# Performance work log

Hardware: AMD Instinct MI355X
Metric: run time of the kernel (lower is better)

## Reference

```python
import jax, jax.numpy as jnp
import numpy as np

N_HEAD, D_MODEL, D_HEAD = 16, 1024, 64
QLEN, BSZ = 1024, 8
LN_EPS = 1e-5


def _rel_shift(x):
    # x: [b, n, i, j]; Transformer-XL relative shift via pad/reshape/slice
    b, n, i, j = x.shape
    x = jnp.pad(x, ((0, 0), (0, 0), (0, 0), (1, 0)))  # [b,n,i,j+1]
    x = x.reshape(b, n, j + 1, i)[:, :, 1:, :].reshape(b, n, i, j)
    return x


def setup_inputs() -> dict:
    key = jax.random.key(0)
    k = jax.random.split(key, 8)
    w = jax.random.normal(k[0], (QLEN, BSZ, D_MODEL), dtype=jnp.float32)
    r_emb = jax.random.normal(k[1], (QLEN, N_HEAD, D_HEAD), dtype=jnp.float32) * 0.02
    r_w_bias = jax.random.normal(k[2], (N_HEAD, D_HEAD), dtype=jnp.float32) * 0.02
    r_bias = jax.random.normal(k[3], (QLEN, N_HEAD), dtype=jnp.float32) * 0.02
    # causal mask: True means masked (j > i)
    attn_mask = jnp.triu(jnp.ones((QLEN, QLEN), dtype=bool), k=1)
    qkv_w = jax.random.normal(k[4], (D_MODEL, 3 * N_HEAD * D_HEAD), dtype=jnp.float32) * (D_MODEL ** -0.5)
    o_w = jax.random.normal(k[5], (N_HEAD * D_HEAD, D_MODEL), dtype=jnp.float32) * ((N_HEAD * D_HEAD) ** -0.5)
    ln_g = jnp.ones((D_MODEL,), dtype=jnp.float32)
    ln_b = jnp.zeros((D_MODEL,), dtype=jnp.float32)
    return {"w": w, "r_emb": r_emb, "r_w_bias": r_w_bias, "r_bias": r_bias,
            "qkv_w": qkv_w, "o_w": o_w, "ln_g": ln_g, "ln_b": ln_b,
            "attn_mask": attn_mask}


def reference(w, r_emb, r_w_bias, r_bias, qkv_w, o_w, ln_g, ln_b, attn_mask):
    qlen, bsz, d_model = w.shape
    n_head, d_head = r_w_bias.shape
    scale = 1.0 / (d_head ** 0.5)

    heads = w @ qkv_w  # [q, b, 3*H*D]
    q_h, k_h, v_h = jnp.split(heads, 3, axis=-1)
    q_h = q_h.reshape(qlen, bsz, n_head, d_head)
    k_h = k_h.reshape(qlen, bsz, n_head, d_head)
    v_h = v_h.reshape(qlen, bsz, n_head, d_head)

    # klen == qlen (no mems), r_emb/r_bias already length klen
    rw_q = q_h + r_w_bias[None, None]                      # [i,b,n,d]
    AC = jnp.einsum('ibnd,jbnd->bnij', rw_q, k_h)          # content score
    B_ = jnp.einsum('ibnd,jnd->bnij', q_h, r_emb)          # position score
    D_ = r_bias.T[None, :, None, :]                        # [1,n,1,j]
    BD = _rel_shift(B_ + D_)
    attn_score = scale * (AC + BD)                         # [b,n,i,j]

    attn_score = jnp.where(attn_mask[None, None], -jnp.inf, attn_score)
    attn_prob = jax.nn.softmax(attn_score, axis=3)

    attn_vec = jnp.einsum('bnij,jbnd->ibnd', attn_prob, v_h)
    attn_vec = attn_vec.reshape(qlen, bsz, n_head * d_head)
    attn_out = attn_vec @ o_w

    # post-LN residual
    y = w + attn_out
    mu = jnp.mean(y, axis=-1, keepdims=True)
    var = jnp.mean((y - mu) ** 2, axis=-1, keepdims=True)
    out = (y - mu) * jax.lax.rsqrt(var + LN_EPS) * ln_g + ln_b
    return out
```

## Files before the change

kernel.cpp:

```cpp
#include <hip/hip_runtime.h>

typedef unsigned short u16;
typedef __attribute__((ext_vector_type(8))) short bf16x8;
typedef __attribute__((ext_vector_type(4))) short bf16x4;
typedef __attribute__((ext_vector_type(4))) float f32x4;
typedef __attribute__((ext_vector_type(4))) unsigned short u16x4;
typedef __attribute__((ext_vector_type(2))) unsigned int u32x2;

#define SEQ 1024
#define BSZ 8
#define NHD 16
#define DHD 64
#define DMODEL 1024

__device__ __forceinline__ u16 f2bf(float x) {
  unsigned u = __float_as_uint(x);
  return (u16)((u + 0x7fffu + ((u >> 16) & 1u)) >> 16);
}
__device__ __forceinline__ float bf2f(u16 h) {
  return __uint_as_float(((unsigned)h) << 16);
}

typedef const __attribute__((address_space(1))) unsigned int gu32_t;
typedef __attribute__((address_space(3))) unsigned int lu32_t;
__device__ __forceinline__ void gload16(const void* g, void* l) {
  __builtin_amdgcn_global_load_lds((gu32_t*)g, (lu32_t*)l, 16, 0, 0);
}

__global__ void cast_w_k(const float* __restrict__ in, u16* __restrict__ out) {
  size_t i = ((size_t)blockIdx.x * 256 + threadIdx.x) * 4;
  float4 v = *(const float4*)(in + i);
  u16x4 o;
  o[0] = f2bf(v.x); o[1] = f2bf(v.y); o[2] = f2bf(v.z); o[3] = f2bf(v.w);
  *(u16x4*)(out + i) = o;
}

__global__ void transpose_cast_k(const float* __restrict__ in, u16* __restrict__ out,
                                 int R, int C) {
  __shared__ float tile[32][33];
  int tx = threadIdx.x & 31, ty = threadIdx.x >> 5;
  int bx = blockIdx.x * 32, by = blockIdx.y * 32;
#pragma unroll
  for (int rr = ty; rr < 32; rr += 8)
    tile[rr][tx] = in[(size_t)(by + rr) * C + bx + tx];
  __syncthreads();
#pragma unroll
  for (int rr = ty; rr < 32; rr += 8)
    out[(size_t)(bx + rr) * R + by + tx] = f2bf(tile[tx][rr]);
}

__global__ void cast_remb_k(const float* __restrict__ in, u16* __restrict__ out) {
  int t0 = blockIdx.x * 256 + threadIdx.x;
  int jn = t0 >> 3, db = t0 & 7;
  int j = jn >> 4, n = jn & 15;
  const float* src = in + (size_t)jn * 64 + db * 8;
  u16* dst = out + (size_t)n * 65536 + (size_t)(j >> 4) * 1024 + (db >> 2) * 512 +
             (((j & 15) | ((db & 3) << 4)) << 3);
#pragma unroll
  for (int e = 0; e < 8; ++e) dst[e] = f2bf(src[e]);
}

__global__ void cvec_k(const float* __restrict__ remb, const float* __restrict__ rwb,
                       float* __restrict__ cv) {
  int idx = blockIdx.x * 256 + threadIdx.x;
  int n = idx >> 10, t = idx & 1023;
  const float* src = remb + (size_t)(t * 16 + n) * 64;
  const float* wb = rwb + n * 64;
  float s = 0.f;
#pragma unroll
  for (int d = 0; d < 64; ++d) s += src[d] * wb[d];
  cv[idx] = s;
}

template <int EPI>
__global__ __launch_bounds__(256) void gemm_bt(
    const u16* __restrict__ A, const u16* __restrict__ Bt, int K, int nbn,
    u16* __restrict__ q_o, u16* __restrict__ k_o, u16* __restrict__ v_o,
    const float* __restrict__ resid, float* __restrict__ yout) {
  __shared__ __attribute__((aligned(16))) u16 ldsA[2][4096];
  __shared__ __attribute__((aligned(16))) u16 ldsB[2][4096];
  const int tid = threadIdx.x;
  const int wid = tid >> 6, l = tid & 63;
  const int l15 = l & 15, lg = l >> 4;
  const int cpx = gridDim.x >> 3;
  const int id0 = blockIdx.x;
  const int lid = (id0 & 7) * cpx + (id0 >> 3);
  const int bm = lid / nbn, bn = lid % nbn;
  const int wm = wid & 1, wn = wid >> 1;
  const size_t ldb = (size_t)K * 2;

  const char* aA = (const char*)A + (size_t)(bm * 128 + wid * 32 + (l >> 2)) * ldb + (l & 3) * 16;
  const char* aB = (const char*)Bt + (size_t)(bn * 128 + wid * 32 + (l >> 2)) * ldb + (l & 3) * 16;

  auto stage = [&](int buf, int kt) {
    const char* sa = aA + (size_t)kt * 64;
    const char* sb = aB + (size_t)kt * 64;
    char* la = (char*)&ldsA[buf][wid * 1024];
    char* lb = (char*)&ldsB[buf][wid * 1024];
    gload16(sa, la);
    gload16(sa + 16 * ldb, la + 1024);
    gload16(sb, lb);
    gload16(sb + 16 * ldb, lb + 1024);
  };

  f32x4 acc[4][4] = {};
  stage(0, 0);
  __syncthreads();
  const int NT = K >> 5;
  for (int t = 0; t < NT; ++t) {
    int cur = t & 1;
    if (t + 1 < NT) stage(cur ^ 1, t + 1);
    bf16x8 af[4], bfr[4];
#pragma unroll
    for (int mi = 0; mi < 4; ++mi)
      af[mi] = *(const bf16x8*)&ldsA[cur][(wm * 64 + mi * 16 + l15) * 32 + lg * 8];
#pragma unroll
    for (int ni = 0; ni < 4; ++ni)
      bfr[ni] = *(const bf16x8*)&ldsB[cur][(wn * 64 + ni * 16 + l15) * 32 + lg * 8];
#pragma unroll
    for (int mi = 0; mi < 4; ++mi)
#pragma unroll
      for (int ni = 0; ni < 4; ++ni)
        acc[mi][ni] = __builtin_amdgcn_mfma_f32_16x16x32_bf16(af[mi], bfr[ni], acc[mi][ni], 0, 0, 0);
    __syncthreads();
  }

  if (EPI == 0) {
#pragma unroll
    for (int mi = 0; mi < 4; ++mi)
#pragma unroll
      for (int ni = 0; ni < 4; ++ni) {
        int c = bn * 128 + wn * 64 + ni * 16 + l15;
        int which = c >> 10, rem = c & 1023, h = rem >> 6, d = rem & 63;
        u16* dst = which == 0 ? q_o : (which == 1 ? k_o : v_o);
#pragma unroll
        for (int r = 0; r < 4; ++r) {
          int rg = bm * 128 + wm * 64 + mi * 16 + lg * 4 + r;
          int i = rg >> 3, bb = rg & 7;
          int bn2 = bb * 16 + h;
          size_t idx;
          if (which == 0) {
            idx = ((size_t)bn2 * 1024 + i) * 64 + d;
          } else if (which == 1) {
            idx = (size_t)bn2 * 65536 + (size_t)(i >> 4) * 1024 + (d >> 5) * 512 +
                  (((i & 15) | (((d >> 3) & 3) << 4)) << 3) + (d & 7);
          } else {
            idx = (size_t)bn2 * 65536 + (size_t)(i >> 4) * 1024 + (d >> 4) * 256 +
                  (((d & 15) | (((i >> 2) & 3) << 4)) << 2) + (i & 3);
          }
          dst[idx] = f2bf(acc[mi][ni][r]);
        }
      }
  } else {
#pragma unroll
    for (int mi = 0; mi < 4; ++mi)
#pragma unroll
      for (int ni = 0; ni < 4; ++ni) {
        int c = bn * 128 + wn * 64 + ni * 16 + l15;
#pragma unroll
        for (int r = 0; r < 4; ++r) {
          int rg = bm * 128 + wm * 64 + mi * 16 + lg * 4 + r;
          size_t off = (size_t)rg * 1024 + c;
          yout[off] = resid[off] + acc[mi][ni][r];
        }
      }
  }
}

__global__ __launch_bounds__(256, 3) void attn_k(
    const u16* __restrict__ qg, const u16* __restrict__ kf, const u16* __restrict__ vf,
    const u16* __restrict__ rf, const float* __restrict__ rbias,
    const float* __restrict__ cvec, const float* __restrict__ rwb,
    u16* __restrict__ av) {
  __shared__ __attribute__((aligned(16))) u16 EldsA[4][16][84];
  __shared__ __attribute__((aligned(16))) u16 EldsB[4][16][84];
  __shared__ __attribute__((aligned(16))) float rb[1088];

  const int tid = threadIdx.x;
  const int wid = tid >> 6, l = tid & 63;
  const int l15 = l & 15, lg = l >> 4;
  const int id = blockIdx.x;
  const int qblk = 7 - (id >> 7);
  const int n = (id & 7) | (((id >> 3) & 1) << 3);
  const int b = (id >> 4) & 7;
  const int bn = b * 16 + n;
  const int ib = qblk * 128;
  const int iw = ib + wid * 32;

  const float SC = 0.18033688011f;

  for (int idx = tid; idx < 1088; idx += 256)
    rb[idx] = (idx < 1024) ? (SC * (rbias[idx * 16 + n] - cvec[n * 1024 + idx]) - 16.0f)
                           : -1e30f;

  const float* wbp = rwb + n * 64;
  const u16* qrowA = qg + ((size_t)bn * 1024 + iw + l15) * 64;
  const u16* qrowB = qrowA + 16 * 64;
  bf16x8 qa0 = *(const bf16x8*)(qrowA + lg * 8);
  bf16x8 qa1 = *(const bf16x8*)(qrowA + 32 + lg * 8);
  bf16x8 qb0 = *(const bf16x8*)(qrowB + lg * 8);
  bf16x8 qb1 = *(const bf16x8*)(qrowB + 32 + lg * 8);
  bf16x8 qwA0, qwA1, qwB0, qwB1;
#pragma unroll
  for (int e = 0; e < 8; ++e) {
    float w0 = wbp[lg * 8 + e], w1 = wbp[32 + lg * 8 + e];
    qwA0[e] = (short)f2bf(SC * (bf2f((u16)qa0[e]) + w0));
    qwA1[e] = (short)f2bf(SC * (bf2f((u16)qa1[e]) + w1));
    qwB0[e] = (short)f2bf(SC * (bf2f((u16)qb0[e]) + w0));
    qwB1[e] = (short)f2bf(SC * (bf2f((u16)qb1[e]) + w1));
  }

  f32x4 oaccA[4] = {}, oaccB[4] = {};
  float lpA = 0.f, lpB = 0.f;

  const u16* kfp = kf + (size_t)bn * 65536 + l * 8;
  const u16* vfp = vf + (size_t)bn * 65536 + l * 4;
  const u16* rfp = rf + (size_t)n * 65536 + l * 8;

  __syncthreads();

  const int njt = (iw >> 6) + 1;
  for (int jt = 0; jt < njt; ++jt) {
    const int jb = jt * 64;

    const u16* kt = kfp + jt * 4096;
    bf16x8 kk[8];
#pragma unroll
    for (int s = 0; s < 8; ++s) kk[s] = *(const bf16x8*)(kt + s * 512);

    const int tbB = jb - iw - 16 + 1008;
    const int t16b = tbB >> 4;
#pragma unroll
    for (int f = 0; f < 6; ++f) {
      int t16 = t16b + f;
      if (t16 > 63) t16 = 63;
      const u16* rr = rfp + t16 * 1024;
      bf16x8 ra0 = *(const bf16x8*)(rr);
      bf16x8 ra1 = *(const bf16x8*)(rr + 512);
      f32x4 rb4 = *(const f32x4*)&rb[tbB + f * 16 + lg * 4];
      if (f < 5) {
        f32x4 et = {};
        et = __builtin_amdgcn_mfma_f32_16x16x32_bf16(ra0, qwB0, et, 0, 0, 0);
        et = __builtin_amdgcn_mfma_f32_16x16x32_bf16(ra1, qwB1, et, 0, 0, 0);
        et = et + rb4;
        unsigned lo, hi;
        asm("v_cvt_pk_bf16_f32 %0, %1, %2" : "=v"(lo) : "v"(et[0]), "v"(et[1]));
        asm("v_cvt_pk_bf16_f32 %0, %1, %2" : "=v"(hi) : "v"(et[2]), "v"(et[3]));
        u32x2 t2; t2[0] = lo; t2[1] = hi;
        *(u32x2*)&EldsB[wid][l15][f * 16 + lg * 4] = t2;
      }
      if (f >= 1) {
        f32x4 et = {};
        et = __builtin_amdgcn_mfma_f32_16x16x32_bf16(ra0, qwA0, et, 0, 0, 0);
        et = __builtin_amdgcn_mfma_f32_16x16x32_bf16(ra1, qwA1, et, 0, 0, 0);
        et = et + rb4;
        unsigned lo, hi;
        asm("v_cvt_pk_bf16_f32 %0, %1, %2" : "=v"(lo) : "v"(et[0]), "v"(et[1]));
        asm("v_cvt_pk_bf16_f32 %0, %1, %2" : "=v"(hi) : "v"(et[2]), "v"(et[3]));
        u32x2 t2; t2[0] = lo; t2[1] = hi;
        *(u32x2*)&EldsA[wid][l15][(f - 1) * 16 + lg * 4] = t2;
      }
    }

    f32x4 stA[4], stB[4];
    __builtin_amdgcn_s_setprio(1);
#pragma unroll
    for (int jj = 0; jj < 4; ++jj) {
      f32x4 a = __builtin_amdgcn_mfma_f32_16x16x32_bf16(kk[jj * 2], qwA0, (f32x4){}, 0, 0, 0);
      stA[jj] = __builtin_amdgcn_mfma_f32_16x16x32_bf16(kk[jj * 2 + 1], qwA1, a, 0, 0, 0);
    }
#pragma unroll
    for (int jj = 0; jj < 4; ++jj) {
      f32x4 a = __builtin_amdgcn_mfma_f32_16x16x32_bf16(kk[jj * 2], qwB0, (f32x4){}, 0, 0, 0);
      stB[jj] = __builtin_amdgcn_mfma_f32_16x16x32_bf16(kk[jj * 2 + 1], qwB1, a, 0, 0, 0);
    }
    __builtin_amdgcn_s_setprio(0);

    const u16* vt0 = vfp + jt * 4096;
    bf16x4 vv[4][4];
#pragma unroll
    for (int jj = 0; jj < 4; ++jj)
#pragma unroll
      for (int dd = 0; dd < 4; ++dd)
        vv[jj][dd] = *(const bf16x4*)(vt0 + jj * 1024 + dd * 256);

    bf16x4 paA[4], paB[4];
#pragma unroll
    for (int jj = 0; jj < 4; ++jj) {
      const int ebase = jj * 16 + lg * 4 - l15 + 15;
      {
        float v0 = stA[jj][0] + bf2f(EldsA[wid][l15][ebase + 0]);
        float v1 = stA[jj][1] + bf2f(EldsA[wid][l15][ebase + 1]);
        float v2 = stA[jj][2] + bf2f(EldsA[wid][l15][ebase + 2]);
        float v3 = stA[jj][3] + bf2f(EldsA[wid][l15][ebase + 3]);
        float p0, p1, p2, p3;
        asm("v_exp_f32 %0, %1" : "=v"(p0) : "v"(v0));
        asm("v_exp_f32 %0, %1" : "=v"(p1) : "v"(v1));
        asm("v_exp_f32 %0, %1" : "=v"(p2) : "v"(v2));
        asm("v_exp_f32 %0, %1" : "=v"(p3) : "v"(v3));
        lpA += (p0 + p1) + (p2 + p3);
        unsigned lo, hi;
        asm("v_cvt_pk_bf16_f32 %0, %1, %2" : "=v"(lo) : "v"(p0), "v"(p1));
        asm("v_cvt_pk_bf16_f32 %0, %1, %2" : "=v"(hi) : "v"(p2), "v"(p3));
        u32x2 t2; t2[0] = lo; t2[1] = hi;
        paA[jj] = __builtin_bit_cast(bf16x4, t2);
      }
      {
        float v0 = stB[jj][0] + bf2f(EldsB[wid][l15][ebase + 0]);
        float v1 = stB[jj][1] + bf2f(EldsB[wid][l15][ebase + 1]);
        float v2 = stB[jj][2] + bf2f(EldsB[wid][l15][ebase + 2]);
        float v3 = stB[jj][3] + bf2f(EldsB[wid][l15][ebase + 3]);
        float p0, p1, p2, p3;
        asm("v_exp_f32 %0, %1" : "=v"(p0) : "v"(v0));
        asm("v_exp_f32 %0, %1" : "=v"(p1) : "v"(v1));
        asm("v_exp_f32 %0, %1" : "=v"(p2) : "v"(v2));
        asm("v_exp_f32 %0, %1" : "=v"(p3) : "v"(v3));
        lpB += (p0 + p1) + (p2 + p3);
        unsigned lo, hi;
        asm("v_cvt_pk_bf16_f32 %0, %1, %2" : "=v"(lo) : "v"(p0), "v"(p1));
        asm("v_cvt_pk_bf16_f32 %0, %1, %2" : "=v"(hi) : "v"(p2), "v"(p3));
        u32x2 t2; t2[0] = lo; t2[1] = hi;
        paB[jj] = __builtin_bit_cast(bf16x4, t2);
      }
    }

    __builtin_amdgcn_s_setprio(1);
#pragma unroll
    for (int dd = 0; dd < 4; ++dd)
#pragma unroll
      for (int jj = 0; jj < 4; ++jj)
        oaccA[dd] = __builtin_amdgcn_mfma_f32_16x16x16bf16_1k(paA[jj], vv[jj][dd], oaccA[dd], 0, 0, 0);
#pragma unroll
    for (int dd = 0; dd < 4; ++dd)
#pragma unroll
      for (int jj = 0; jj < 4; ++jj)
        oaccB[dd] = __builtin_amdgcn_mfma_f32_16x16x16bf16_1k(paB[jj], vv[jj][dd], oaccB[dd], 0, 0, 0);
    __builtin_amdgcn_s_setprio(0);
  }

  lpA += __shfl_xor(lpA, 16);
  lpA += __shfl_xor(lpA, 32);
  lpB += __shfl_xor(lpB, 16);
  lpB += __shfl_xor(lpB, 32);
  float liA = 1.f / lpA, liB = 1.f / lpB;
  float ioA[4], ioB[4];
#pragma unroll
  for (int r2 = 0; r2 < 4; ++r2) {
    ioA[r2] = __shfl(liA, (l & 48) | (lg * 4 + r2));
    ioB[r2] = __shfl(liB, (l & 48) | (lg * 4 + r2));
  }
#pragma unroll
  for (int dd = 0; dd < 4; ++dd)
#pragma unroll
    for (int r2 = 0; r2 < 4; ++r2) {
      int igA = iw + lg * 4 + r2;
      av[((size_t)igA * 8 + b) * 1024 + n * 64 + dd * 16 + l15] = f2bf(oaccA[dd][r2] * ioA[r2]);
      int igB = igA + 16;
      av[((size_t)igB * 8 + b) * 1024 + n * 64 + dd * 16 + l15] = f2bf(oaccB[dd][r2] * ioB[r2]);
    }
}

__global__ void ln_k(float* __restrict__ y, const float* __restrict__ g,
                     const float* __restrict__ be) {
  const int row = blockIdx.x, tid = threadIdx.x;
  float* p = y + (size_t)row * 1024;
  float4 v = ((const float4*)p)[tid];
  float s1 = v.x + v.y + v.z + v.w;
  float s2 = v.x * v.x + v.y * v.y + v.z * v.z + v.w * v.w;
#pragma unroll
  for (int mk = 1; mk < 64; mk <<= 1) {
    s1 += __shfl_xor(s1, mk);
    s2 += __shfl_xor(s2, mk);
  }
  __shared__ float as1[4], as2[4];
  if ((tid & 63) == 0) { as1[tid >> 6] = s1; as2[tid >> 6] = s2; }
  __syncthreads();
  s1 = as1[0] + as1[1] + as1[2] + as1[3];
  s2 = as2[0] + as2[1] + as2[2] + as2[3];
  float mu = s1 * (1.f / 1024.f);
  float var = s2 * (1.f / 1024.f) - mu * mu;
  float rs = rsqrtf(var + 1e-5f);
  float4 gg = ((const float4*)g)[tid];
  float4 bb = ((const float4*)be)[tid];
  float4 o;
  o.x = (v.x - mu) * rs * gg.x + bb.x;
  o.y = (v.y - mu) * rs * gg.y + bb.y;
  o.z = (v.z - mu) * rs * gg.z + bb.z;
  o.w = (v.w - mu) * rs * gg.w + bb.w;
  ((float4*)p)[tid] = o;
}

extern "C" void kernel_launch(void* const* d_in, const int* in_sizes, int n_in,
                              void* d_out, int out_size, void* d_ws, size_t ws_size,
                              hipStream_t stream) {
  (void)in_sizes; (void)n_in; (void)out_size; (void)ws_size;
  const float* w      = (const float*)d_in[0];
  const float* r_emb  = (const float*)d_in[1];
  const float* r_wb   = (const float*)d_in[2];
  const float* r_bias = (const float*)d_in[3];
  const float* qkv_w  = (const float*)d_in[4];
  const float* o_w    = (const float*)d_in[5];
  const float* ln_g   = (const float*)d_in[6];
  const float* ln_b   = (const float*)d_in[7];
  float* out = (float*)d_out;
  char* ws = (char*)d_ws;

  u16* w_b    = (u16*)(ws + 0);
  u16* qkvw_t = (u16*)(ws + 16777216);
  u16* ow_t   = (u16*)(ws + 23068672);
  u16* remb_f = (u16*)(ws + 25165824);
  u16* q_b    = (u16*)(ws + 27262976);
  u16* k_f    = (u16*)(ws + 44040192);
  u16* v_f    = (u16*)(ws + 60817408);
  float* cvb  = (float*)(ws + 77594624);
  u16* av_b   = w_b;

  cast_w_k<<<8192, 256, 0, stream>>>(w, w_b);
  transpose_cast_k<<<dim3(96, 32), 256, 0, stream>>>(qkv_w, qkvw_t, 1024, 3072);
  transpose_cast_k<<<dim3(32, 32), 256, 0, stream>>>(o_w, ow_t, 1024, 1024);
  cast_remb_k<<<512, 256, 0, stream>>>(r_emb, remb_f);
  cvec_k<<<64, 256, 0, stream>>>(r_emb, r_wb, cvb);
  gemm_bt<0><<<dim3(1536), 256, 0, stream>>>(w_b, qkvw_t, 1024, 24, q_b, k_f, v_f, nullptr, nullptr);
  attn_k<<<dim3(1024), 256, 0, stream>>>(q_b, k_f, v_f, remb_f, r_bias, cvb, r_wb, av_b);
  gemm_bt<1><<<dim3(512), 256, 0, stream>>>(av_b, ow_t, 1024, 8, nullptr, nullptr, nullptr, w, out);
  ln_k<<<8192, 256, 0, stream>>>(out, ln_g, ln_b);
}
```

Measured before the change: 199.4 us.

## Fuse preprocessing kernels into one launch and halve attention block size

Merges the five preprocessing kernels (w cast, two weight transpose-casts, r_emb relayout, cvec dot products) into a single launch that dispatches on block index, cutting launch overhead and inter-kernel gaps. The attention kernel now uses 128-thread blocks covering 64 query rows with 2048 blocks instead of 256 threads over 128 rows. The smaller blocks give finer load balance across the causal triangle and more resident blocks, but each block redoes the r_bias table setup, and the hidden body must handle two waves correctly.

```diff
diff --git a/kernel.cpp b/kernel.cpp
--- a/kernel.cpp
+++ b/kernel.cpp
@@ -27,49 +27,56 @@
   __builtin_amdgcn_global_load_lds((gu32_t*)g, (lu32_t*)l, 16, 0, 0);
 }
 
-__global__ void cast_w_k(const float* __restrict__ in, u16* __restrict__ out) {
-  size_t i = ((size_t)blockIdx.x * 256 + threadIdx.x) * 4;
-  float4 v = *(const float4*)(in + i);
-  u16x4 o;
-  o[0] = f2bf(v.x); o[1] = f2bf(v.y); o[2] = f2bf(v.z); o[3] = f2bf(v.w);
-  *(u16x4*)(out + i) = o;
-}
-
-__global__ void transpose_cast_k(const float* __restrict__ in, u16* __restrict__ out,
-                                 int R, int C) {
+__global__ void prep_k(const float* __restrict__ w, const float* __restrict__ qkv_w,
+                       const float* __restrict__ o_w, const float* __restrict__ r_emb,
+                       const float* __restrict__ rwb,
+                       u16* __restrict__ w_b, u16* __restrict__ qkvw_t,
+                       u16* __restrict__ ow_t, u16* __restrict__ remb_f,
+                       float* __restrict__ cvb) {
   __shared__ float tile[32][33];
-  int tx = threadIdx.x & 31, ty = threadIdx.x >> 5;
-  int bx = blockIdx.x * 32, by = blockIdx.y * 32;
-#pragma unroll
-  for (int rr = ty; rr < 32; rr += 8)
-    tile[rr][tx] = in[(size_t)(by + rr) * C + bx + tx];
-  __syncthreads();
-#pragma unroll
-  for (int rr = ty; rr < 32; rr += 8)
-    out[(size_t)(bx + rr) * R + by + tx] = f2bf(tile[tx][rr]);
-}
-
-__global__ void cast_remb_k(const float* __restrict__ in, u16* __restrict__ out) {
-  int t0 = blockIdx.x * 256 + threadIdx.x;
-  int jn = t0 >> 3, db = t0 & 7;
-  int j = jn >> 4, n = jn & 15;
-  const float* src = in + (size_t)jn * 64 + db * 8;
-  u16* dst = out + (size_t)n * 65536 + (size_t)(j >> 4) * 1024 + (db >> 2) * 512 +
-             (((j & 15) | ((db & 3) << 4)) << 3);
-#pragma unroll
-  for (int e = 0; e < 8; ++e) dst[e] = f2bf(src[e]);
-}
-
-__global__ void cvec_k(const float* __restrict__ remb, const float* __restrict__ rwb,
-                       float* __restrict__ cv) {
-  int idx = blockIdx.x * 256 + threadIdx.x;
-  int n = idx >> 10, t = idx & 1023;
-  const float* src = remb + (size_t)(t * 16 + n) * 64;
-  const float* wb = rwb + n * 64;
-  float s = 0.f;
-#pragma unroll
-  for (int d = 0; d < 64; ++d) s += src[d] * wb[d];
-  cv[idx] = s;
+  const int id = blockIdx.x;
+  const int tid = threadIdx.x;
+  if (id < 8192) {
+    size_t i = ((size_t)id * 256 + tid) * 4;
+    float4 v = *(const float4*)(w + i);
+    u16x4 o;
+    o[0] = f2bf(v.x); o[1] = f2bf(v.y); o[2] = f2bf(v.z); o[3] = f2bf(v.w);
+    *(u16x4*)(w_b + i) = o;
+  } else if (id < 12288) {
+    const bool isq = id < 11264;
+    const int lid = isq ? (id - 8192) : (id - 11264);
+    const int C = isq ? 3072 : 1024;
+    const int bx = (isq ? (lid % 96) : (lid & 31)) * 32;
+    const int by = (isq ? (lid / 96) : (lid >> 5)) * 32;
+    const float* in = isq ? qkv_w : o_w;
+    u16* out = isq ? qkvw_t : ow_t;
+    const int tx = tid & 31, ty = tid >> 5;
+#pragma unroll
+    for (int rr = ty; rr < 32; rr += 8)
+      tile[rr][tx] = in[(size_t)(by + rr) * C + bx + tx];
+    __syncthreads();
+#pragma unroll
+    for (int rr = ty; rr < 32; rr += 8)
+      out[(size_t)(bx + rr) * 1024 + by + tx] = f2bf(tile[tx][rr]);
+  } else if (id < 12800) {
+    int t0 = (id - 12288) * 256 + tid;
+    int jn = t0 >> 3, db = t0 & 7;
+    int j = jn >> 4, n = jn & 15;
+    const float* src = r_emb + (size_t)jn * 64 + db * 8;
+    u16* dst = remb_f + (size_t)n * 65536 + (size_t)(j >> 4) * 1024 + (db >> 2) * 512 +
+               (((j & 15) | ((db & 3) << 4)) << 3);
+#pragma unroll
+    for (int e = 0; e < 8; ++e) dst[e] = f2bf(src[e]);
+  } else {
+    int idx = (id - 12800) * 256 + tid;
+    int n = idx >> 10, t = idx & 1023;
+    const float* src = r_emb + (size_t)(t * 16 + n) * 64;
+    const float* wb = rwb + n * 64;
+    float s = 0.f;
+#pragma unroll
+    for (int d = 0; d < 64; ++d) s += src[d] * wb[d];
+    cvb[idx] = s;
+  }
 }
 
 template <int EPI>
@@ -167,29 +174,29 @@
   }
 }
 
-__global__ __launch_bounds__(256, 3) void attn_k(
+__global__ __launch_bounds__(128, 3) void attn_k(
     const u16* __restrict__ qg, const u16* __restrict__ kf, const u16* __restrict__ vf,
     const u16* __restrict__ rf, const float* __restrict__ rbias,
     const float* __restrict__ cvec, const float* __restrict__ rwb,
     u16* __restrict__ av) {
-  __shared__ __attribute__((aligned(16))) u16 EldsA[4][16][84];
-  __shared__ __attribute__((aligned(16))) u16 EldsB[4][16][84];
+  __shared__ __attribute__((aligned(16))) u16 EldsA[2][16][84];
+  __shared__ __attribute__((aligned(16))) u16 EldsB[2][16][84];
   __shared__ __attribute__((aligned(16))) float rb[1088];
 
   const int tid = threadIdx.x;
   const int wid = tid >> 6, l = tid & 63;
   const int l15 = l & 15, lg = l >> 4;
   const int id = blockIdx.x;
-  const int qblk = 7 - (id >> 7);
+  const int qblk = 15 - (id >> 7);
   const int n = (id & 7) | (((id >> 3) & 1) << 3);
   const int b = (id >> 4) & 7;
   const int bn = b * 16 + n;
-  const int ib = qblk * 128;
+  const int ib = qblk * 64;
   const int iw = ib + wid * 32;
 
   const float SC = 0.18033688011f;
 
-  for (int idx = tid; idx < 1088; idx += 256)
+  for (int idx = tid; idx < 1088; idx += 128)
     rb[idx] = (idx < 1024) ? (SC * (rbias[idx * 16 + n] - cvec[n * 1024 + idx]) - 16.0f)
                            : -1e30f;
 
@@ -415,13 +422,10 @@
   float* cvb  = (float*)(ws + 77594624);
   u16* av_b   = w_b;
 
-  cast_w_k<<<8192, 256, 0, stream>>>(w, w_b);
-  transpose_cast_k<<<dim3(96, 32), 256, 0, stream>>>(qkv_w, qkvw_t, 1024, 3072);
-  transpose_cast_k<<<dim3(32, 32), 256, 0, stream>>>(o_w, ow_t, 1024, 1024);
-  cast_remb_k<<<512, 256, 0, stream>>>(r_emb, remb_f);
-  cvec_k<<<64, 256, 0, stream>>>(r_emb, r_wb, cvb);
+  prep_k<<<dim3(12864), 256, 0, stream>>>(w, qkv_w, o_w, r_emb, r_wb,
+                                          w_b, qkvw_t, ow_t, remb_f, cvb);
   gemm_bt<0><<<dim3(1536), 256, 0, stream>>>(w_b, qkvw_t, 1024, 24, q_b, k_f, v_f, nullptr, nullptr);
-  attn_k<<<dim3(1024), 256, 0, stream>>>(q_b, k_f, v_f, remb_f, r_bias, cvb, r_wb, av_b);
+  attn_k<<<dim3(2048), 128, 0, stream>>>(q_b, k_f, v_f, remb_f, r_bias, cvb, r_wb, av_b);
   gemm_bt<1><<<dim3(512), 256, 0, stream>>>(av_b, ow_t, 1024, 8, nullptr, nullptr, nullptr, w, out);
   ln_k<<<8192, 256, 0, stream>>>(out, ln_g, ln_b);
 }
```

Result: faster. 193.9 us (-2.7%).
